# Performance work log

Measured on AMD Instinct MI355X. Metric: run time of the kernel, lower is better.

The kernel has to match this reference:

```python
import jax, jax.numpy as jnp
import numpy as np

E, H, L, DFF, PF = 256, 8, 6, 1024, 6

def _ln(x, s, b):
    m = x.mean(-1, keepdims=True)
    v = jnp.mean((x - m) ** 2, -1, keepdims=True)
    return (x - m) / jnp.sqrt(v + 1e-5) * s + b

def _gelu(x):
    return jax.nn.gelu(x, approximate=False)

def setup_inputs() -> dict:
    key = jax.random.key(0)
    ks = iter(jax.random.split(key, 40))
    B, N = 16, 512
    w = lambda shape: jax.random.normal(next(ks), shape, jnp.float32) * 0.02
    hits = jax.random.normal(next(ks), (B, N, 5), jnp.float32)
    mask = jax.random.uniform(next(ks), (B, N)) < 0.9
    mask = mask.at[:, 0].set(True)  # at least one valid hit per event
    params = jax.random.normal(next(ks), (B, 5), jnp.float32)
    return dict(
        hits=hits, mask=mask, params=params,
        embed_w=w((5, E)), embed_b=jnp.zeros(E), embed_ln_s=jnp.ones(E), embed_ln_b=jnp.zeros(E),
        pos_w=w((2, E)), pos_b=jnp.zeros(E),
        qkv_w=w((L, E, 3 * E)), out_w=w((L, E, E)), out_b=jnp.zeros((L, E)),
        pair_w1=w((L, PF, E)), pair_b1=jnp.zeros((L, E)), pair_w2=w((L, E, H)), pair_b2=jnp.zeros((L, H)),
        ffn_w1=w((L, E, DFF)), ffn_b1=jnp.zeros((L, DFF)), ffn_w2=w((L, DFF, E)), ffn_b2=jnp.zeros((L, E)),
        n1_s=jnp.ones((L, E)), n1_b=jnp.zeros((L, E)), n2_s=jnp.ones((L, E)), n2_b=jnp.zeros((L, E)),
        pfc_w1=w((5, E)), pfc_b1=jnp.zeros(E), pfc_ln_s=jnp.ones(E), pfc_ln_b=jnp.zeros(E),
        pfc_w2=w((E, E)), pfc_b2=jnp.zeros(E),
        cls_w1=w((3 * E, 512)), cls_b1=jnp.zeros(512),
        cls_w2=w((512, 256)), cls_b2=jnp.zeros(256),
        cls_w3=w((256, 2)), cls_b3=jnp.zeros(2))

def reference(hits, mask, params, embed_w, embed_b, embed_ln_s, embed_ln_b, pos_w, pos_b,
              qkv_w, out_w, out_b, pair_w1, pair_b1, pair_w2, pair_b2,
              ffn_w1, ffn_b1, ffn_w2, ffn_b2, n1_s, n1_b, n2_s, n2_b,
              pfc_w1, pfc_b1, pfc_ln_s, pfc_ln_b, pfc_w2, pfc_b2,
              cls_w1, cls_b1, cls_w2, cls_b2, cls_w3, cls_b3):
    B, N, _ = hits.shape
    pos = hits[..., :2]
    feat = _gelu(_ln(hits @ embed_w + embed_b, embed_ln_s, embed_ln_b)) + _gelu(pos @ pos_w + pos_b)

    # pairwise geometric features [B,N,N,5]
    d = hits[:, :, None, :] - hits[:, None, :, :]
    dx, dy, dr, dpe, ddt = (d[..., i] for i in range(5))
    dist = jnp.sqrt(dx * dx + dy * dy + 1e-6)
    nrm = lambda t: t / (jnp.mean(jnp.abs(t), axis=(1, 2), keepdims=True) + 1e-6)
    dist_n = dist / (jnp.mean(dist, axis=(1, 2), keepdims=True) + 1e-6)
    pair_feat = jnp.stack([nrm(dx), nrm(dy), dist_n, nrm(dr), nrm(dpe), nrm(ddt)], axis=-1)

    Dh = feat.shape[-1] // H
    scale = Dh ** -0.5
    key_mask = mask[:, None, None, :]  # [B,1,1,N]
    for l in range(qkv_w.shape[0]):
        q, k, v = jnp.split(feat @ qkv_w[l], 3, axis=-1)
        q = q.reshape(B, N, H, Dh)
        k = k.reshape(B, N, H, Dh)
        v = v.reshape(B, N, H, Dh)
        logits = jnp.einsum('bqhd,bkhd->bhqk', q, k) * scale
        bias = jax.nn.relu(pair_feat @ pair_w1[l] + pair_b1[l]) @ pair_w2[l] + pair_b2[l]  # [B,N,N,H]
        logits = logits + jnp.transpose(bias, (0, 3, 1, 2))
        logits = jnp.where(key_mask, logits, -1e9)
        attn = jax.nn.softmax(logits, axis=-1)
        out = jnp.einsum('bhqk,bkhd->bqhd', attn, v).reshape(B, N, -1)
        out = out @ out_w[l] + out_b[l]
        x = _ln(feat + out, n1_s[l], n1_b[l])
        x2 = _gelu(x @ ffn_w1[l] + ffn_b1[l]) @ ffn_w2[l] + ffn_b2[l]
        feat = _ln(x + x2, n2_s[l], n2_b[l])

    mask_f = mask[..., None].astype(feat.dtype)
    mean_feat = (feat * mask_f).sum(1) / (mask_f.sum(1) + 1e-6)
    max_feat = jnp.where(mask[..., None], feat, -1e9).max(1)
    invalid = mask.sum(1) == 0
    max_feat = jnp.where(invalid[:, None], mean_feat, max_feat)

    pf = _gelu(params @ pfc_w1 + pfc_b1)
    pf = _ln(pf, pfc_ln_s, pfc_ln_b)
    pf = _gelu(pf @ pfc_w2 + pfc_b2)

    h = jnp.concatenate([max_feat, mean_feat, pf], axis=1)
    h = _gelu(h @ cls_w1 + cls_b1)
    h = _gelu(h @ cls_w2 + cls_b2)
    return h @ cls_w3 + cls_b3
```

## Files before the change

### kernel.cpp

```cpp
#include <hip/hip_runtime.h>
#include <hip/hip_bf16.h>

#define B_ 16
#define N_ 512
#define E_ 256
#define H_ 8
#define DH_ 32
#define L_ 6
#define DFF_ 1024
#define LSN 528

typedef unsigned short ushort_t;
typedef __attribute__((ext_vector_type(8))) short short8v;
typedef __attribute__((ext_vector_type(4))) float f32x4;

__device__ __forceinline__ float bf2f_raw(unsigned short u){
    unsigned int x = ((unsigned int)u) << 16; float f;
    __builtin_memcpy(&f, &x, 4); return f;
}
__device__ __forceinline__ unsigned short f2bf_rne(float f){
    unsigned int u; __builtin_memcpy(&u, &f, 4);
    u += 0x7fffu + ((u >> 16) & 1u);
    return (unsigned short)(u >> 16);
}
__device__ __forceinline__ unsigned int packbf2(float a, float b){
    return (unsigned int)f2bf_rne(a) | ((unsigned int)f2bf_rne(b) << 16);
}
__device__ __forceinline__ unsigned int pack_hi16(float a, float b){
    unsigned int ua, ub;
    __builtin_memcpy(&ua, &a, 4); __builtin_memcpy(&ub, &b, 4);
    return __builtin_amdgcn_perm(ub, ua, 0x07060302);
}
__device__ __forceinline__ float gelu_f(float x){
    return 0.5f * x * (1.0f + erff(x * 0.7071067811865476f));
}

__global__ void detect_and_mask(const unsigned int* __restrict__ lnS_raw,
                                const void* __restrict__ mask_raw,
                                int* __restrict__ flag, int* __restrict__ maskI){
    __shared__ int s_isbf, s_m32;
    if (threadIdx.x == 0){
        s_isbf = (lnS_raw[0] == 0x3F803F80u) ? 1 : 0;
        const unsigned int* mw = (const unsigned int*)mask_raw;
        int ok = 1;
        for (int k = 0; k < 64; k++){ if (mw[k] > 1u){ ok = 0; break; } }
        s_m32 = ok;
        *flag = s_isbf;
    }
    __syncthreads();
    if (s_m32){
        const int* mi = (const int*)mask_raw;
        for (int i = threadIdx.x; i < B_*N_; i += blockDim.x) maskI[i] = (mi[i] != 0);
    } else {
        const unsigned char* mb = (const unsigned char*)mask_raw;
        for (int i = threadIdx.x; i < B_*N_; i += blockDim.x) maskI[i] = (mb[i] != 0);
    }
}

struct CvtTable {
    const void* src[36];
    int off[37];
    int dstoff[36];
};

__global__ __launch_bounds__(256) void cvt_all(CvtTable t, float* __restrict__ base,
                                               const int* __restrict__ flag){
    int gi = blockIdx.x * 256 + threadIdx.x;
    if (gi >= t.off[36]) return;
    int seg = 0;
    for (int s = 1; s < 36; s++) if (gi >= t.off[s]) seg = s;
    int loc = gi - t.off[seg];
    float* dst = base + t.dstoff[seg] + loc;
    if (*flag) *dst = bf2f_raw(((const unsigned short*)t.src[seg])[loc]);
    else       *dst = ((const float*)t.src[seg])[loc];
}

struct TPTable {
    const float* src[24];
    ushort_t* dst[24];
    int K[24], N[24];
    int tile0[25];
};

__global__ __launch_bounds__(256) void wpack(TPTable tp){
    int bid = blockIdx.x;
    int m = 0;
    while (m + 1 < 24 && bid >= tp.tile0[m+1]) m++;
    int t = bid - tp.tile0[m];
    int tiles_n = tp.N[m] >> 5;
    int tk = t / tiles_n, tn = t - tk*tiles_n;
    __shared__ float tile[32][33];
    int tx = threadIdx.x & 31, ty = threadIdx.x >> 5;
    const float* src = tp.src[m];
    int Nn = tp.N[m], Kk = tp.K[m];
    #pragma unroll
    for (int r = 0; r < 4; r++){
        int k = tk*32 + ty + r*8;
        tile[ty + r*8][tx] = src[(size_t)k*Nn + tn*32 + tx];
    }
    __syncthreads();
    ushort_t* dst = tp.dst[m];
    #pragma unroll
    for (int r = 0; r < 4; r++){
        int n = tn*32 + ty + r*8;
        dst[(size_t)n*Kk + tk*32 + tx] = f2bf_rne(tile[tx][ty + r*8]);
    }
}

__global__ __launch_bounds__(256) void pair_stats(const float* __restrict__ hits,
                                                  float* __restrict__ ppart){
    int blk = blockIdx.x;
    int b = blk >> 5, chunk = blk & 31;
    int tid = threadIdx.x;
    float acc[6] = {0,0,0,0,0,0};
    for (int ii = 0; ii < 16; ii++){
        int i = chunk*16 + ii;
        const float* hi = hits + (size_t)(b*N_ + i)*5;
        float h0=hi[0], h1=hi[1], h2=hi[2], h3=hi[3], h4=hi[4];
        for (int j = tid; j < N_; j += 256){
            const float* hj = hits + (size_t)(b*N_ + j)*5;
            float dx = h0 - hj[0], dy = h1 - hj[1];
            acc[0] += fabsf(dx);
            acc[1] += fabsf(dy);
            acc[2] += sqrtf(dx*dx + dy*dy + 1e-6f);
            acc[3] += fabsf(h2 - hj[2]);
            acc[4] += fabsf(h3 - hj[3]);
            acc[5] += fabsf(h4 - hj[4]);
        }
    }
    __shared__ float red[256];
    for (int c = 0; c < 6; c++){
        red[tid] = acc[c]; __syncthreads();
        for (int s = 128; s > 0; s >>= 1){ if (tid < s) red[tid] += red[tid+s]; __syncthreads(); }
        if (tid == 0) ppart[(size_t)(b*32 + chunk)*6 + c] = red[0];
        __syncthreads();
    }
}

__global__ void pair_fin(const float* __restrict__ ppart, float* __restrict__ pscale){
    int t = threadIdx.x;
    if (t >= B_*6) return;
    int b = t / 6, c = t % 6;
    float s = 0.f;
    for (int k = 0; k < 32; k++) s += ppart[(size_t)(b*32 + k)*6 + c];
    float mean = s * (1.0f / (float)(N_*N_));
    pscale[t] = 1.0f / (mean + 1e-6f);
}

__global__ __launch_bounds__(256) void embed_kernel(const float* __restrict__ hits,
        const float* __restrict__ ew, const float* __restrict__ eb,
        const float* __restrict__ lns, const float* __restrict__ lnb,
        const float* __restrict__ pw, const float* __restrict__ pb,
        float* __restrict__ feat, ushort_t* __restrict__ featb){
    int row = blockIdx.x; int e = threadIdx.x;
    const float* h = hits + (size_t)row*5;
    float h0=h[0], h1=h[1], h2=h[2], h3=h[3], h4=h[4];
    float t = eb[e] + h0*ew[e] + h1*ew[E_+e] + h2*ew[2*E_+e] + h3*ew[3*E_+e] + h4*ew[4*E_+e];
    __shared__ float red[256];
    red[e] = t; __syncthreads();
    for (int s = 128; s > 0; s >>= 1){ if (e < s) red[e] += red[e+s]; __syncthreads(); }
    float m = red[0] * (1.0f/E_); __syncthreads();
    float d = t - m;
    red[e] = d*d; __syncthreads();
    for (int s = 128; s > 0; s >>= 1){ if (e < s) red[e] += red[e+s]; __syncthreads(); }
    float v = red[0] * (1.0f/E_);
    float ln = d * rsqrtf(v + 1e-5f) * lns[e] + lnb[e];
    float g1 = gelu_f(ln);
    float p = pb[e] + h0*pw[e] + h1*pw[E_+e];
    float o = g1 + gelu_f(p);
    feat[(size_t)row*E_ + e] = o;
    featb[(size_t)row*E_ + e] = f2bf_rne(o);
}

template<int ACT>
__global__ __launch_bounds__(256) void gemm_bf16(const ushort_t* __restrict__ A,
        const ushort_t* __restrict__ WT, const float* __restrict__ bias,
        float* __restrict__ C, ushort_t* __restrict__ Cbf, int M, int Ncols, int K){
    __shared__ __align__(16) ushort_t As[64][72];
    __shared__ __align__(16) ushort_t Bs[64][72];
    int tid = threadIdx.x;
    int mBase = blockIdx.y * 64, nBase = blockIdx.x * 64;
    int l = tid & 63, w = tid >> 6;
    int l15 = l & 15, lg = l >> 4;
    int wm = w >> 1, wn = w & 1;
    int srow = tid >> 2, skq = (tid & 3) * 16;
    f32x4 acc00 = {0.f,0.f,0.f,0.f}, acc01 = acc00, acc10 = acc00, acc11 = acc00;
    for (int kt = 0; kt < K; kt += 64){
        uint4 av0 = *(const uint4*)(A  + (size_t)(mBase+srow)*K + kt + skq);
        uint4 av1 = *(const uint4*)(A  + (size_t)(mBase+srow)*K + kt + skq + 8);
        uint4 bv0 = *(const uint4*)(WT + (size_t)(nBase+srow)*K + kt + skq);
        uint4 bv1 = *(const uint4*)(WT + (size_t)(nBase+srow)*K + kt + skq + 8);
        *(uint4*)&As[srow][skq]     = av0;
        *(uint4*)&As[srow][skq + 8] = av1;
        *(uint4*)&Bs[srow][skq]     = bv0;
        *(uint4*)&Bs[srow][skq + 8] = bv1;
        __syncthreads();
        #pragma unroll
        for (int ks = 0; ks < 2; ks++){
            short8v a0 = *(short8v*)&As[wm*32      + l15][ks*32 + lg*8];
            short8v a1 = *(short8v*)&As[wm*32 + 16 + l15][ks*32 + lg*8];
            short8v b0 = *(short8v*)&Bs[wn*32      + l15][ks*32 + lg*8];
            short8v b1 = *(short8v*)&Bs[wn*32 + 16 + l15][ks*32 + lg*8];
            acc00 = __builtin_amdgcn_mfma_f32_16x16x32_bf16(a0, b0, acc00, 0, 0, 0);
            acc01 = __builtin_amdgcn_mfma_f32_16x16x32_bf16(a0, b1, acc01, 0, 0, 0);
            acc10 = __builtin_amdgcn_mfma_f32_16x16x32_bf16(a1, b0, acc10, 0, 0, 0);
            acc11 = __builtin_amdgcn_mfma_f32_16x16x32_bf16(a1, b1, acc11, 0, 0, 0);
        }
        __syncthreads();
    }
    #pragma unroll
    for (int fm = 0; fm < 2; fm++){
        #pragma unroll
        for (int fn = 0; fn < 2; fn++){
            f32x4 a = (fm==0) ? ((fn==0)?acc00:acc01) : ((fn==0)?acc10:acc11);
            int col = nBase + wn*32 + fn*16 + l15;
            float bs = bias ? bias[col] : 0.f;
            #pragma unroll
            for (int r = 0; r < 4; r++){
                int row = mBase + wm*32 + fm*16 + lg*4 + r;
                float o = a[r] + bs;
                if (ACT == 1) o = gelu_f(o);
                if (C)   C[(size_t)row*Ncols + col] = o;
                if (Cbf) Cbf[(size_t)row*Ncols + col] = f2bf_rne(o);
            }
        }
    }
}

__global__ __launch_bounds__(128) void pk_pack(const float* __restrict__ qkv,
        const float* __restrict__ hits, const float* __restrict__ pscale,
        const float* __restrict__ w1, unsigned int* __restrict__ PTbf,
        unsigned int* __restrict__ Kbf){
    int row = blockIdx.x;
    int b = row >> 9;
    int t = threadIdx.x;
    const float* sc6 = pscale + b*6;
    const float* h = hits + (size_t)row*5;
    float a0 = h[0]*sc6[0], a1 = h[1]*sc6[1], a2 = h[2]*sc6[3], a3 = h[3]*sc6[4], a4 = h[4]*sc6[5];
    int c0 = t*2;
    float p0 = a0*w1[c0]   + a1*w1[E_+c0]   + a2*w1[3*E_+c0]   + a3*w1[4*E_+c0]   + a4*w1[5*E_+c0];
    float p1 = a0*w1[c0+1] + a1*w1[E_+c0+1] + a2*w1[3*E_+c0+1] + a3*w1[4*E_+c0+1] + a4*w1[5*E_+c0+1];
    PTbf[(size_t)row*128 + t] = packbf2(p0, p1);
    const float* kr = qkv + (size_t)row*768 + 256 + c0;
    Kbf[(size_t)row*128 + t] = packbf2(kr[0], kr[1]);
}

__device__ __forceinline__ short8v build_afrag(uint4 pt, float4 b0, float4 b1,
                                               float4 w0, float4 w1v, float dist){
    float p0 = bf2f_raw((ushort_t)(pt.x & 0xffff)), p1 = bf2f_raw((ushort_t)(pt.x >> 16));
    float p2 = bf2f_raw((ushort_t)(pt.y & 0xffff)), p3 = bf2f_raw((ushort_t)(pt.y >> 16));
    float p4 = bf2f_raw((ushort_t)(pt.z & 0xffff)), p5 = bf2f_raw((ushort_t)(pt.z >> 16));
    float p6 = bf2f_raw((ushort_t)(pt.w & 0xffff)), p7 = bf2f_raw((ushort_t)(pt.w >> 16));
    float e0 = fmaxf(fmaf(dist, w0.x,  b0.x - p0), 0.f);
    float e1 = fmaxf(fmaf(dist, w0.y,  b0.y - p1), 0.f);
    float e2 = fmaxf(fmaf(dist, w0.z,  b0.z - p2), 0.f);
    float e3 = fmaxf(fmaf(dist, w0.w,  b0.w - p3), 0.f);
    float e4 = fmaxf(fmaf(dist, w1v.x, b1.x - p4), 0.f);
    float e5 = fmaxf(fmaf(dist, w1v.y, b1.y - p5), 0.f);
    float e6 = fmaxf(fmaf(dist, w1v.z, b1.z - p6), 0.f);
    float e7 = fmaxf(fmaf(dist, w1v.w, b1.w - p7), 0.f);
    uint4 u;
    u.x = pack_hi16(e0, e1); u.y = pack_hi16(e2, e3);
    u.z = pack_hi16(e4, e5); u.w = pack_hi16(e6, e7);
    return *(short8v*)&u;
}

__global__ __launch_bounds__(512, 4) void attn7_kernel(
        const float* __restrict__ qkv, const unsigned int* __restrict__ PTbf,
        const unsigned int* __restrict__ Kbf, const float* __restrict__ hits,
        const int* __restrict__ maskI, const float* __restrict__ pscale,
        const float* __restrict__ b1, const float* __restrict__ w1,
        const float* __restrict__ w2, const float* __restrict__ b2,
        ushort_t* __restrict__ attnob){
    __shared__ __align__(16) ushort_t Ls[2][H_][LSN];
    __shared__ __align__(16) float4 w2f[8][64];
    __shared__ float baseS[2][E_];
    __shared__ float w1dS[E_];
    __shared__ float distS[2][N_];
    __shared__ unsigned char mS[N_];
    __shared__ float b2S[8];
    __shared__ float red[512];
    __shared__ float inv_s[2][H_];

    int bx = blockIdx.x;
    int b = bx >> 8;
    int i0 = (bx & 255) * 2;
    int tid = threadIdx.x;
    int l = tid & 63, w = tid >> 6;
    int l15 = l & 15, lg = l >> 4;
    const float scale = 0.17677669529663687f;

    {
        int q = tid >> 8, c = tid & 255;
        const float* sc6 = pscale + b*6;
        const float* hr = hits + (size_t)(b*N_ + i0 + q)*5;
        float p = hr[0]*sc6[0]*w1[c] + hr[1]*sc6[1]*w1[E_+c] + hr[2]*sc6[3]*w1[3*E_+c]
                + hr[3]*sc6[4]*w1[4*E_+c] + hr[4]*sc6[5]*w1[5*E_+c];
        baseS[q][c] = p + b1[c];
        if (tid < 256) w1dS[tid] = sc6[2] * w1[2*E_ + tid];
        if (tid < 8)   b2S[tid] = b2[tid];
    }
    {
        int ks = tid >> 6, lv = tid & 63;
        int h = lv & 15, g = lv >> 4;
        uint4 u = {0u,0u,0u,0u};
        if (h < 8){
            int cb = ks*32 + g*8;
            const float* wp = w2 + (size_t)cb*H_ + h;
            u.x = packbf2(wp[0*H_], wp[1*H_]);
            u.y = packbf2(wp[2*H_], wp[3*H_]);
            u.z = packbf2(wp[4*H_], wp[5*H_]);
            u.w = packbf2(wp[6*H_], wp[7*H_]);
        }
        w2f[ks][lv] = *(float4*)&u;
    }
    for (int idx = tid; idx < 1024; idx += 512){
        int q = idx >> 9, j = idx & 511;
        const float* hi = hits + (size_t)(b*N_ + i0 + q)*5;
        const float* hj = hits + (size_t)(b*N_ + j)*5;
        float dx = hi[0] - hj[0], dy = hi[1] - hj[1];
        distS[q][j] = sqrtf(dx*dx + dy*dy + 1e-6f);
        if (q == 0) mS[j] = (unsigned char)(maskI[b*N_ + j] != 0);
    }
    uint4 qz = {0u,0u,0u,0u};
    short8v zero8 = *(short8v*)&qz;
    short8v qreg0 = zero8, qreg1 = zero8;
    if (l15 < 8){
        const float* Q0 = qkv + (size_t)(b*N_ + i0    )*768 + l15*32 + lg*8;
        const float* Q1 = qkv + (size_t)(b*N_ + i0 + 1)*768 + l15*32 + lg*8;
        uint4 u0, u1;
        u0.x = packbf2(Q0[0]*scale, Q0[1]*scale); u0.y = packbf2(Q0[2]*scale, Q0[3]*scale);
        u0.z = packbf2(Q0[4]*scale, Q0[5]*scale); u0.w = packbf2(Q0[6]*scale, Q0[7]*scale);
        u1.x = packbf2(Q1[0]*scale, Q1[1]*scale); u1.y = packbf2(Q1[2]*scale, Q1[3]*scale);
        u1.z = packbf2(Q1[4]*scale, Q1[5]*scale); u1.w = packbf2(Q1[6]*scale, Q1[7]*scale);
        qreg0 = *(short8v*)&u0; qreg1 = *(short8v*)&u1;
    }
    __syncthreads();

    int jb = w << 6;
    int j0 = jb + l15;
    const unsigned int* PTb = PTbf + (size_t)b*N_*128;
    const unsigned int* Kb  = Kbf  + (size_t)b*N_*128;
    f32x4 a00 = {0.f,0.f,0.f,0.f}, a01 = a00, a02 = a00, a03 = a00;
    f32x4 a10 = a00, a11 = a00, a12 = a00, a13 = a00;
    float d00 = distS[0][j0], d01 = distS[0][j0+16], d02 = distS[0][j0+32], d03 = distS[0][j0+48];
    float d10 = distS[1][j0], d11 = distS[1][j0+16], d12 = distS[1][j0+32], d13 = distS[1][j0+48];

    #pragma unroll
    for (int ks = 0; ks < 8; ks++){
        int cbase = ks*32 + lg*8;
        float4 wfrag4 = w2f[ks][l];
        short8v wfrag = *(short8v*)&wfrag4;
        float4 w0  = *(float4*)&w1dS[cbase];
        float4 w1v = *(float4*)&w1dS[cbase + 4];
        uint4 pt0 = *(const uint4*)(PTb + (size_t)(j0      )*128 + (cbase >> 1));
        uint4 pt1 = *(const uint4*)(PTb + (size_t)(j0 + 16 )*128 + (cbase >> 1));
        uint4 pt2 = *(const uint4*)(PTb + (size_t)(j0 + 32 )*128 + (cbase >> 1));
        uint4 pt3 = *(const uint4*)(PTb + (size_t)(j0 + 48 )*128 + (cbase >> 1));
        {
            float4 bs0 = *(float4*)&baseS[0][cbase];
            float4 bs1 = *(float4*)&baseS[0][cbase + 4];
            short8v f0 = build_afrag(pt0, bs0, bs1, w0, w1v, d00);
            short8v f1 = build_afrag(pt1, bs0, bs1, w0, w1v, d01);
            short8v f2 = build_afrag(pt2, bs0, bs1, w0, w1v, d02);
            short8v f3 = build_afrag(pt3, bs0, bs1, w0, w1v, d03);
            a00 = __builtin_amdgcn_mfma_f32_16x16x32_bf16(f0, wfrag, a00, 0, 0, 0);
            a01 = __builtin_amdgcn_mfma_f32_16x16x32_bf16(f1, wfrag, a01, 0, 0, 0);
            a02 = __builtin_amdgcn_mfma_f32_16x16x32_bf16(f2, wfrag, a02, 0, 0, 0);
            a03 = __builtin_amdgcn_mfma_f32_16x16x32_bf16(f3, wfrag, a03, 0, 0, 0);
        }
        {
            float4 bs0 = *(float4*)&baseS[1][cbase];
            float4 bs1 = *(float4*)&baseS[1][cbase + 4];
            short8v f0 = build_afrag(pt0, bs0, bs1, w0, w1v, d10);
            short8v f1 = build_afrag(pt1, bs0, bs1, w0, w1v, d11);
            short8v f2 = build_afrag(pt2, bs0, bs1, w0, w1v, d12);
            short8v f3 = build_afrag(pt3, bs0, bs1, w0, w1v, d13);
            a10 = __builtin_amdgcn_mfma_f32_16x16x32_bf16(f0, wfrag, a10, 0, 0, 0);
            a11 = __builtin_amdgcn_mfma_f32_16x16x32_bf16(f1, wfrag, a11, 0, 0, 0);
            a12 = __builtin_amdgcn_mfma_f32_16x16x32_bf16(f2, wfrag, a12, 0, 0, 0);
            a13 = __builtin_amdgcn_mfma_f32_16x16x32_bf16(f3, wfrag, a13, 0, 0, 0);
        }
    }
    #pragma unroll
    for (int ks = 0; ks < 8; ks++){
        int dbase = ks*32 + lg*8;
        short8v q0f = (l15 == ks) ? qreg0 : zero8;
        short8v q1f = (l15 == ks) ? qreg1 : zero8;
        uint4 k0 = *(const uint4*)(Kb + (size_t)(j0      )*128 + (dbase >> 1));
        uint4 k1 = *(const uint4*)(Kb + (size_t)(j0 + 16 )*128 + (dbase >> 1));
        uint4 k2 = *(const uint4*)(Kb + (size_t)(j0 + 32 )*128 + (dbase >> 1));
        uint4 k3 = *(const uint4*)(Kb + (size_t)(j0 + 48 )*128 + (dbase >> 1));
        short8v kf0 = *(short8v*)&k0, kf1 = *(short8v*)&k1, kf2 = *(short8v*)&k2, kf3 = *(short8v*)&k3;
        a00 = __builtin_amdgcn_mfma_f32_16x16x32_bf16(kf0, q0f, a00, 0, 0, 0);
        a01 = __builtin_amdgcn_mfma_f32_16x16x32_bf16(kf1, q0f, a01, 0, 0, 0);
        a02 = __builtin_amdgcn_mfma_f32_16x16x32_bf16(kf2, q0f, a02, 0, 0, 0);
        a03 = __builtin_amdgcn_mfma_f32_16x16x32_bf16(kf3, q0f, a03, 0, 0, 0);
        a10 = __builtin_amdgcn_mfma_f32_16x16x32_bf16(kf0, q1f, a10, 0, 0, 0);
        a11 = __builtin_amdgcn_mfma_f32_16x16x32_bf16(kf1, q1f, a11, 0, 0, 0);
        a12 = __builtin_amdgcn_mfma_f32_16x16x32_bf16(kf2, q1f, a12, 0, 0, 0);
        a13 = __builtin_amdgcn_mfma_f32_16x16x32_bf16(kf3, q1f, a13, 0, 0, 0);
    }

    if (l15 < 8){
        float b2h = b2S[l15];
        ushort_t neg = f2bf_rne(-1e9f);
        #pragma unroll
        for (int r = 0; r < 4; r++){
            int jr0 = jb +  0 + lg*4 + r;
            int jr1 = jb + 16 + lg*4 + r;
            int jr2 = jb + 32 + lg*4 + r;
            int jr3 = jb + 48 + lg*4 + r;
            Ls[0][l15][jr0] = mS[jr0] ? f2bf_rne(a00[r] + b2h) : neg;
            Ls[0][l15][jr1] = mS[jr1] ? f2bf_rne(a01[r] + b2h) : neg;
            Ls[0][l15][jr2] = mS[jr2] ? f2bf_rne(a02[r] + b2h) : neg;
            Ls[0][l15][jr3] = mS[jr3] ? f2bf_rne(a03[r] + b2h) : neg;
            Ls[1][l15][jr0] = mS[jr0] ? f2bf_rne(a10[r] + b2h) : neg;
            Ls[1][l15][jr1] = mS[jr1] ? f2bf_rne(a11[r] + b2h) : neg;
            Ls[1][l15][jr2] = mS[jr2] ? f2bf_rne(a12[r] + b2h) : neg;
            Ls[1][l15][jr3] = mS[jr3] ? f2bf_rne(a13[r] + b2h) : neg;
        }
    }
    __syncthreads();

    {
        int g = tid >> 5, lane = tid & 31;
        int sq = g >> 3, shh = g & 7;
        ushort_t* Li = &Ls[sq][shh][0];
        float m = -3e38f;
        for (int jj = lane; jj < N_; jj += 32) m = fmaxf(m, bf2f_raw(Li[jj]));
        red[tid] = m; __syncthreads();
        #pragma unroll
        for (int s = 16; s > 0; s >>= 1){ if (lane < s) red[tid] = fmaxf(red[tid], red[tid+s]); __syncthreads(); }
        float mh = red[g << 5]; __syncthreads();
        float ss = 0.f;
        for (int jj = lane; jj < N_; jj += 32){
            float e = __expf(bf2f_raw(Li[jj]) - mh);
            ushort_t us = f2bf_rne(e);
            Li[jj] = us;
            ss += bf2f_raw(us);
        }
        red[tid] = ss; __syncthreads();
        #pragma unroll
        for (int s = 16; s > 0; s >>= 1){ if (lane < s) red[tid] += red[tid+s]; __syncthreads(); }
        if (lane == 0) inv_s[sq][shh] = 1.0f / red[g << 5];
        __syncthreads();
    }

    {
        int q = tid >> 8, d = tid & 255, hh = d >> 5;
        const float* vb = qkv + (size_t)(b*N_)*768 + 512 + d;
        const uint4* Lp = (const uint4*)&Ls[q][hh][0];
        float o = 0.f;
        for (int jb2 = 0; jb2 < N_/8; jb2++){
            uint4 ww = Lp[jb2];
            int j0b = jb2*8;
            unsigned int wk[4] = {ww.x, ww.y, ww.z, ww.w};
            #pragma unroll
            for (int k = 0; k < 4; k++){
                unsigned int lo = wk[k] << 16;
                unsigned int hi = wk[k] & 0xffff0000u;
                float plo, phi;
                __builtin_memcpy(&plo, &lo, 4);
                __builtin_memcpy(&phi, &hi, 4);
                o = fmaf(plo, vb[(size_t)(j0b + 2*k    )*768], o);
                o = fmaf(phi, vb[(size_t)(j0b + 2*k + 1)*768], o);
            }
        }
        attnob[(size_t)(b*N_ + i0 + q)*E_ + d] = f2bf_rne(o * inv_s[q][hh]);
    }
}

__global__ __launch_bounds__(256) void ln_add_kernel(const float* __restrict__ a,
        const float* __restrict__ bsrc, const float* __restrict__ s,
        const float* __restrict__ bb, float* __restrict__ out,
        ushort_t* __restrict__ outb){
    int row = blockIdx.x, e = threadIdx.x;
    float v = a[(size_t)row*E_ + e] + bsrc[(size_t)row*E_ + e];
    __shared__ float red[256];
    red[e] = v; __syncthreads();
    for (int t = 128; t > 0; t >>= 1){ if (e < t) red[e] += red[e+t]; __syncthreads(); }
    float m = red[0] * (1.0f/E_); __syncthreads();
    float d = v - m;
    red[e] = d*d; __syncthreads();
    for (int t = 128; t > 0; t >>= 1){ if (e < t) red[e] += red[e+t]; __syncthreads(); }
    float var = red[0] * (1.0f/E_);
    float o = d * rsqrtf(var + 1e-5f) * s[e] + bb[e];
    out[(size_t)row*E_ + e] = o;
    outb[(size_t)row*E_ + e] = f2bf_rne(o);
}

__global__ __launch_bounds__(256) void pool_kernel(const float* __restrict__ feat,
        const int* __restrict__ maskI, float* __restrict__ pooled){
    int b = blockIdx.x, e = threadIdx.x;
    __shared__ int ml[N_];
    for (int n = e; n < N_; n += 256) ml[n] = maskI[b*N_ + n];
    __syncthreads();
    float s = 0.f, mx = -1e30f; int cnt = 0;
    for (int n = 0; n < N_; n++){
        if (ml[n]){
            float v = feat[(size_t)(b*N_ + n)*E_ + e];
            s += v; mx = fmaxf(mx, v); cnt++;
        }
    }
    float mean = s / ((float)cnt + 1e-6f);
    if (cnt == 0) mx = mean;
    pooled[b*768 + e]       = mx;
    pooled[b*768 + 256 + e] = mean;
}

__global__ __launch_bounds__(256) void pf_kernel(const float* __restrict__ params,
        const float* __restrict__ w1, const float* __restrict__ b1,
        const float* __restrict__ lns, const float* __restrict__ lnb,
        const float* __restrict__ w2, const float* __restrict__ b2,
        float* __restrict__ pooled){
    int b = blockIdx.x, e = threadIdx.x;
    __shared__ float red[256];
    __shared__ float pfn[256];
    float p0 = params[b*5+0], p1 = params[b*5+1], p2 = params[b*5+2], p3 = params[b*5+3], p4 = params[b*5+4];
    float t = b1[e] + p0*w1[e] + p1*w1[E_+e] + p2*w1[2*E_+e] + p3*w1[3*E_+e] + p4*w1[4*E_+e];
    t = gelu_f(t);
    red[e] = t; __syncthreads();
    for (int s = 128; s > 0; s >>= 1){ if (e < s) red[e] += red[e+s]; __syncthreads(); }
    float m = red[0] * (1.0f/E_); __syncthreads();
    float d = t - m;
    red[e] = d*d; __syncthreads();
    for (int s = 128; s > 0; s >>= 1){ if (e < s) red[e] += red[e+s]; __syncthreads(); }
    float v = red[0] * (1.0f/E_);
    pfn[e] = d * rsqrtf(v + 1e-5f) * lns[e] + lnb[e];
    __syncthreads();
    float u = b2[e];
    for (int c = 0; c < E_; c++) u += pfn[c] * w2[c*E_ + e];
    pooled[b*768 + 512 + e] = gelu_f(u);
}

__global__ __launch_bounds__(512) void cls_kernel(const float* __restrict__ pooled,
        const float* __restrict__ w1, const float* __restrict__ b1,
        const float* __restrict__ w2, const float* __restrict__ b2,
        const float* __restrict__ w3, const float* __restrict__ b3,
        float* __restrict__ out){
    int b = blockIdx.x, t = threadIdx.x;
    __shared__ float hb[768];
    __shared__ float h1[512];
    __shared__ float h2[256];
    for (int idx = t; idx < 768; idx += 512) hb[idx] = pooled[b*768 + idx];
    __syncthreads();
    float a = b1[t];
    for (int c = 0; c < 768; c++) a += hb[c] * w1[c*512 + t];
    h1[t] = gelu_f(a);
    __syncthreads();
    if (t < 256){
        float a2 = b2[t];
        for (int c = 0; c < 512; c++) a2 += h1[c] * w2[c*256 + t];
        h2[t] = gelu_f(a2);
    }
    __syncthreads();
    if (t < 2){
        float a3 = b3[t];
        for (int c = 0; c < 256; c++) a3 += h2[c] * w3[c*2 + t];
        out[b*2 + t] = a3;
    }
}

extern "C" void kernel_launch(void* const* d_in, const int* in_sizes, int n_in,
                              void* d_out, int out_size, void* d_ws, size_t ws_size,
                              hipStream_t stream){
    enum { I_HITS=0, I_MASK=1, I_PARAMS=2, I_EMBED_W=3, I_EMBED_B=4, I_ELN_S=5, I_ELN_B=6,
           I_POS_W=7, I_POS_B=8, I_QKV_W=9, I_OUT_W=10, I_OUT_B=11, I_PW1=12, I_PB1=13,
           I_PW2=14, I_PB2=15, I_FW1=16, I_FB1=17, I_FW2=18, I_FB2=19, I_N1S=20, I_N1B=21,
           I_N2S=22, I_N2B=23, I_PFW1=24, I_PFB1=25, I_PFLS=26, I_PFLB=27, I_PFW2=28, I_PFB2=29,
           I_CW1=30, I_CB1=31, I_CW2=32, I_CB2=33, I_CW3=34, I_CB3=35 };
    (void)n_in; (void)out_size; (void)ws_size;

    float* wsf = (float*)d_ws;
    int* maskI = (int*)d_ws;
    int* flag  = (int*)d_ws + 8192;
    size_t off = 8448;

    CvtTable tbl;
    float* cv[36];
    for (int idx = 0; idx < 36; idx++){
        if (idx == I_MASK){ cv[idx] = nullptr; tbl.src[idx] = d_in[idx]; tbl.dstoff[idx] = 0; continue; }
        cv[idx] = wsf + off;
        tbl.src[idx] = d_in[idx];
        tbl.dstoff[idx] = (int)off;
        off += (size_t)in_sizes[idx];
        off = (off + 3) & ~(size_t)3;
    }
    {
        int c2 = 0;
        for (int idx = 0; idx < 36; idx++){
            tbl.off[idx] = c2;
            if (idx != I_MASK) c2 += in_sizes[idx];
        }
        tbl.off[36] = c2;
    }

    float* feat  = wsf + off; off += (size_t)B_*N_*E_;
    float* qkv   = wsf + off; off += (size_t)B_*N_*3*E_;
    float* xbuf  = wsf + off; off += (size_t)B_*N_*E_;
    float* tmp   = wsf + off; off += (size_t)B_*N_*E_;
    float* ppart = wsf + off; off += (size_t)B_*32*6;
    float* pscale= wsf + off; off += (size_t)B_*6 + 2;
    float* pooled= wsf + off; off += (size_t)B_*768;
    ushort_t* featb  = (ushort_t*)(wsf + off); off += (size_t)B_*N_*E_/2;
    ushort_t* xbufb  = (ushort_t*)(wsf + off); off += (size_t)B_*N_*E_/2;
    ushort_t* attnob = (ushort_t*)(wsf + off); off += (size_t)B_*N_*E_/2;
    ushort_t* ffnhb  = (ushort_t*)(wsf + off); off += (size_t)B_*N_*DFF_/2;
    ushort_t* wtq = (ushort_t*)(wsf + off); off += (size_t)L_*768*E_/2;
    ushort_t* wto = (ushort_t*)(wsf + off); off += (size_t)L_*E_*E_/2;
    ushort_t* wt1 = (ushort_t*)(wsf + off); off += (size_t)L_*DFF_*E_/2;
    ushort_t* wt2 = (ushort_t*)(wsf + off); off += (size_t)L_*E_*DFF_/2;
    unsigned int* PTbf = (unsigned int*)tmp;
    unsigned int* Kbf  = PTbf + (size_t)B_*N_*128;

    detect_and_mask<<<1, 256, 0, stream>>>((const unsigned int*)d_in[I_ELN_S], d_in[I_MASK], flag, maskI);
    {
        int total = tbl.off[36];
        cvt_all<<<(total + 255)/256, 256, 0, stream>>>(tbl, wsf, flag);
    }

    {
        TPTable tp;
        int t0 = 0;
        for (int l = 0; l < L_; l++){
            int m = l*4;
            tp.src[m+0] = cv[I_QKV_W] + (size_t)l*E_*3*E_; tp.dst[m+0] = wtq + (size_t)l*768*E_;
            tp.K[m+0] = E_;   tp.N[m+0] = 3*E_;
            tp.src[m+1] = cv[I_OUT_W] + (size_t)l*E_*E_;   tp.dst[m+1] = wto + (size_t)l*E_*E_;
            tp.K[m+1] = E_;   tp.N[m+1] = E_;
            tp.src[m+2] = cv[I_FW1] + (size_t)l*E_*DFF_;   tp.dst[m+2] = wt1 + (size_t)l*DFF_*E_;
            tp.K[m+2] = E_;   tp.N[m+2] = DFF_;
            tp.src[m+3] = cv[I_FW2] + (size_t)l*DFF_*E_;   tp.dst[m+3] = wt2 + (size_t)l*E_*DFF_;
            tp.K[m+3] = DFF_; tp.N[m+3] = E_;
        }
        for (int m = 0; m < 24; m++){
            tp.tile0[m] = t0;
            t0 += (tp.K[m] >> 5) * (tp.N[m] >> 5);
        }
        tp.tile0[24] = t0;
        wpack<<<t0, 256, 0, stream>>>(tp);
    }

    pair_stats<<<B_*32, 256, 0, stream>>>(cv[I_HITS], ppart);
    pair_fin<<<1, 128, 0, stream>>>(ppart, pscale);
    embed_kernel<<<B_*N_, 256, 0, stream>>>(cv[I_HITS], cv[I_EMBED_W], cv[I_EMBED_B],
                                            cv[I_ELN_S], cv[I_ELN_B], cv[I_POS_W], cv[I_POS_B],
                                            feat, featb);

    for (int l = 0; l < L_; l++){
        gemm_bf16<0><<<dim3(12,128), 256, 0, stream>>>(featb, wtq + (size_t)l*768*E_,
                                                       nullptr, qkv, nullptr, B_*N_, 3*E_, E_);
        pk_pack<<<B_*N_, 128, 0, stream>>>(qkv, cv[I_HITS], pscale,
                                           cv[I_PW1] + (size_t)l*6*E_, PTbf, Kbf);
        attn7_kernel<<<B_*(N_/2), 512, 0, stream>>>(qkv, PTbf, Kbf, cv[I_HITS], maskI, pscale,
                                               cv[I_PB1] + (size_t)l*E_,
                                               cv[I_PW1] + (size_t)l*6*E_,
                                               cv[I_PW2] + (size_t)l*E_*H_,
                                               cv[I_PB2] + (size_t)l*H_,
                                               attnob);
        gemm_bf16<0><<<dim3(4,128), 256, 0, stream>>>(attnob, wto + (size_t)l*E_*E_,
                                                      cv[I_OUT_B] + (size_t)l*E_, tmp, nullptr,
                                                      B_*N_, E_, E_);
        ln_add_kernel<<<B_*N_, 256, 0, stream>>>(feat, tmp, cv[I_N1S] + (size_t)l*E_,
                                                 cv[I_N1B] + (size_t)l*E_, xbuf, xbufb);
        gemm_bf16<1><<<dim3(16,128), 256, 0, stream>>>(xbufb, wt1 + (size_t)l*DFF_*E_,
                                                       cv[I_FB1] + (size_t)l*DFF_, nullptr, ffnhb,
                                                       B_*N_, DFF_, E_);
        gemm_bf16<0><<<dim3(4,128), 256, 0, stream>>>(ffnhb, wt2 + (size_t)l*E_*DFF_,
                                                      cv[I_FB2] + (size_t)l*E_, tmp, nullptr,
                                                      B_*N_, E_, DFF_);
        ln_add_kernel<<<B_*N_, 256, 0, stream>>>(xbuf, tmp, cv[I_N2S] + (size_t)l*E_,
                                                 cv[I_N2B] + (size_t)l*E_, feat, featb);
    }

    pool_kernel<<<B_, 256, 0, stream>>>(feat, maskI, pooled);
    pf_kernel<<<B_, 256, 0, stream>>>(cv[I_PARAMS], cv[I_PFW1], cv[I_PFB1],
                                      cv[I_PFLS], cv[I_PFLB], cv[I_PFW2], cv[I_PFB2], pooled);
    cls_kernel<<<B_, 512, 0, stream>>>(pooled, cv[I_CW1], cv[I_CB1], cv[I_CW2], cv[I_CB2],
                                       cv[I_CW3], cv[I_CB3], (float*)d_out);
}
```

Before: 3.388 ms.

## Switch pair-bias MLP to packed fp16 math and transpose V to fp16

The pair-bias hidden layer is now computed with packed half2 FMA/max instead of per-element fp32 ops plus bf16 packing, and uses fp16 MFMA. Attention logits and probabilities are stored as fp16. A new vT_pack kernel writes a transposed fp16 copy of V, so the PV accumulation does contiguous vector loads with fdot2 instead of strided fp32 gathers. This cuts ALU and memory traffic in the attention kernel. It adds an extra kernel launch per layer and risks fp16 range and precision problems in the intermediate values.

```diff
diff --git a/kernel.cpp b/kernel.cpp
--- a/kernel.cpp
+++ b/kernel.cpp
@@ -1,5 +1,6 @@
 #include <hip/hip_runtime.h>
 #include <hip/hip_bf16.h>
+#include <hip/hip_fp16.h>
 
 #define B_ 16
 #define N_ 512
@@ -13,6 +14,8 @@
 typedef unsigned short ushort_t;
 typedef __attribute__((ext_vector_type(8))) short short8v;
 typedef __attribute__((ext_vector_type(4))) float f32x4;
+typedef __attribute__((ext_vector_type(2))) _Float16 half2v;
+typedef __attribute__((ext_vector_type(8))) _Float16 half8v;
 
 __device__ __forceinline__ float bf2f_raw(unsigned short u){
     unsigned int x = ((unsigned int)u) << 16; float f;
@@ -26,10 +29,24 @@
 __device__ __forceinline__ unsigned int packbf2(float a, float b){
     return (unsigned int)f2bf_rne(a) | ((unsigned int)f2bf_rne(b) << 16);
 }
-__device__ __forceinline__ unsigned int pack_hi16(float a, float b){
-    unsigned int ua, ub;
-    __builtin_memcpy(&ua, &a, 4); __builtin_memcpy(&ub, &b, 4);
-    return __builtin_amdgcn_perm(ub, ua, 0x07060302);
+__device__ __forceinline__ half2v u2hv(unsigned int u){ half2v h; __builtin_memcpy(&h, &u, 4); return h; }
+__device__ __forceinline__ unsigned int hv2u(half2v h){ unsigned int u; __builtin_memcpy(&u, &h, 4); return u; }
+__device__ __forceinline__ unsigned int pack2h(float a, float b){
+    half2v h; h.x = (_Float16)a; h.y = (_Float16)b; return hv2u(h);
+}
+__device__ __forceinline__ ushort_t f2h_u(float f){
+    _Float16 h = (_Float16)f; ushort_t u; __builtin_memcpy(&u, &h, 2); return u;
+}
+__device__ __forceinline__ float h2f_u(ushort_t u){
+    _Float16 h; __builtin_memcpy(&h, &u, 2); return (float)h;
+}
+__device__ __forceinline__ float dot2h(unsigned int p, unsigned int v, float c){
+#if __has_builtin(__builtin_amdgcn_fdot2)
+    return __builtin_amdgcn_fdot2(u2hv(p), u2hv(v), c, false);
+#else
+    half2v a = u2hv(p), b = u2hv(v);
+    return fmaf((float)a.y, (float)b.y, fmaf((float)a.x, (float)b.x, c));
+#endif
 }
 __device__ __forceinline__ float gelu_f(float x){
     return 0.5f * x * (1.0f + erff(x * 0.7071067811865476f));
@@ -104,6 +121,25 @@
     for (int r = 0; r < 4; r++){
         int n = tn*32 + ty + r*8;
         dst[(size_t)n*Kk + tk*32 + tx] = f2bf_rne(tile[tx][ty + r*8]);
+    }
+}
+
+__global__ __launch_bounds__(256) void vT_pack(const float* __restrict__ qkv,
+                                               ushort_t* __restrict__ VTf){
+    __shared__ float t[32][33];
+    int b = blockIdx.z;
+    int n0 = blockIdx.x * 32, d0 = blockIdx.y * 32;
+    int tx = threadIdx.x & 31, ty = threadIdx.x >> 5;
+    #pragma unroll
+    for (int r = 0; r < 4; r++){
+        int n = ty + r*8;
+        t[n][tx] = qkv[(size_t)(b*N_ + n0 + n)*768 + 512 + d0 + tx];
+    }
+    __syncthreads();
+    #pragma unroll
+    for (int r = 0; r < 4; r++){
+        int d = ty + r*8;
+        VTf[(size_t)(b*E_ + d0 + d)*N_ + n0 + tx] = f2h_u(t[tx][d]);
     }
 }
 
@@ -229,7 +265,7 @@
 
 __global__ __launch_bounds__(128) void pk_pack(const float* __restrict__ qkv,
         const float* __restrict__ hits, const float* __restrict__ pscale,
-        const float* __restrict__ w1, unsigned int* __restrict__ PTbf,
+        const float* __restrict__ w1, unsigned int* __restrict__ PThf,
         unsigned int* __restrict__ Kbf){
     int row = blockIdx.x;
     int b = row >> 9;
@@ -240,42 +276,38 @@
     int c0 = t*2;
     float p0 = a0*w1[c0]   + a1*w1[E_+c0]   + a2*w1[3*E_+c0]   + a3*w1[4*E_+c0]   + a4*w1[5*E_+c0];
     float p1 = a0*w1[c0+1] + a1*w1[E_+c0+1] + a2*w1[3*E_+c0+1] + a3*w1[4*E_+c0+1] + a4*w1[5*E_+c0+1];
-    PTbf[(size_t)row*128 + t] = packbf2(p0, p1);
+    PThf[(size_t)row*128 + t] = pack2h(p0, p1);
     const float* kr = qkv + (size_t)row*768 + 256 + c0;
     Kbf[(size_t)row*128 + t] = packbf2(kr[0], kr[1]);
 }
 
-__device__ __forceinline__ short8v build_afrag(uint4 pt, float4 b0, float4 b1,
-                                               float4 w0, float4 w1v, float dist){
-    float p0 = bf2f_raw((ushort_t)(pt.x & 0xffff)), p1 = bf2f_raw((ushort_t)(pt.x >> 16));
-    float p2 = bf2f_raw((ushort_t)(pt.y & 0xffff)), p3 = bf2f_raw((ushort_t)(pt.y >> 16));
-    float p4 = bf2f_raw((ushort_t)(pt.z & 0xffff)), p5 = bf2f_raw((ushort_t)(pt.z >> 16));
-    float p6 = bf2f_raw((ushort_t)(pt.w & 0xffff)), p7 = bf2f_raw((ushort_t)(pt.w >> 16));
-    float e0 = fmaxf(fmaf(dist, w0.x,  b0.x - p0), 0.f);
-    float e1 = fmaxf(fmaf(dist, w0.y,  b0.y - p1), 0.f);
-    float e2 = fmaxf(fmaf(dist, w0.z,  b0.z - p2), 0.f);
-    float e3 = fmaxf(fmaf(dist, w0.w,  b0.w - p3), 0.f);
-    float e4 = fmaxf(fmaf(dist, w1v.x, b1.x - p4), 0.f);
-    float e5 = fmaxf(fmaf(dist, w1v.y, b1.y - p5), 0.f);
-    float e6 = fmaxf(fmaf(dist, w1v.z, b1.z - p6), 0.f);
-    float e7 = fmaxf(fmaf(dist, w1v.w, b1.w - p7), 0.f);
+__device__ __forceinline__ half8v build_afrag_h(uint4 pt, uint4 bs, uint4 wd, half2v d2){
+    half2v z2 = (half2v)(_Float16)0;
+    half2v r0 = d2 * u2hv(wd.x) + (u2hv(bs.x) - u2hv(pt.x));
+    half2v r1 = d2 * u2hv(wd.y) + (u2hv(bs.y) - u2hv(pt.y));
+    half2v r2 = d2 * u2hv(wd.z) + (u2hv(bs.z) - u2hv(pt.z));
+    half2v r3 = d2 * u2hv(wd.w) + (u2hv(bs.w) - u2hv(pt.w));
+    r0 = __builtin_elementwise_max(r0, z2);
+    r1 = __builtin_elementwise_max(r1, z2);
+    r2 = __builtin_elementwise_max(r2, z2);
+    r3 = __builtin_elementwise_max(r3, z2);
     uint4 u;
-    u.x = pack_hi16(e0, e1); u.y = pack_hi16(e2, e3);
-    u.z = pack_hi16(e4, e5); u.w = pack_hi16(e6, e7);
-    return *(short8v*)&u;
-}
-
-__global__ __launch_bounds__(512, 4) void attn7_kernel(
-        const float* __restrict__ qkv, const unsigned int* __restrict__ PTbf,
-        const unsigned int* __restrict__ Kbf, const float* __restrict__ hits,
+    u.x = hv2u(r0); u.y = hv2u(r1); u.z = hv2u(r2); u.w = hv2u(r3);
+    half8v r; __builtin_memcpy(&r, &u, 16); return r;
+}
+
+__global__ __launch_bounds__(512, 4) void attn8_kernel(
+        const float* __restrict__ qkv, const unsigned int* __restrict__ PThf,
+        const unsigned int* __restrict__ Kbf, const ushort_t* __restrict__ VTf,
+        const float* __restrict__ hits,
         const int* __restrict__ maskI, const float* __restrict__ pscale,
         const float* __restrict__ b1, const float* __restrict__ w1,
         const float* __restrict__ w2, const float* __restrict__ b2,
         ushort_t* __restrict__ attnob){
     __shared__ __align__(16) ushort_t Ls[2][H_][LSN];
-    __shared__ __align__(16) float4 w2f[8][64];
-    __shared__ float baseS[2][E_];
-    __shared__ float w1dS[E_];
+    __shared__ __align__(16) uint4 w2f[8][64];
+    __shared__ __align__(16) unsigned int baseH[2][128];
+    __shared__ __align__(16) unsigned int w1dH[128];
     __shared__ float distS[2][N_];
     __shared__ unsigned char mS[N_];
     __shared__ float b2S[8];
@@ -290,15 +322,21 @@
     int l15 = l & 15, lg = l >> 4;
     const float scale = 0.17677669529663687f;
 
-    {
-        int q = tid >> 8, c = tid & 255;
+    if (tid < 256){
+        int q = tid >> 7, cp = tid & 127;
+        int c = cp*2;
         const float* sc6 = pscale + b*6;
         const float* hr = hits + (size_t)(b*N_ + i0 + q)*5;
-        float p = hr[0]*sc6[0]*w1[c] + hr[1]*sc6[1]*w1[E_+c] + hr[2]*sc6[3]*w1[3*E_+c]
-                + hr[3]*sc6[4]*w1[4*E_+c] + hr[4]*sc6[5]*w1[5*E_+c];
-        baseS[q][c] = p + b1[c];
-        if (tid < 256) w1dS[tid] = sc6[2] * w1[2*E_ + tid];
-        if (tid < 8)   b2S[tid] = b2[tid];
+        float pa = hr[0]*sc6[0]*w1[c] + hr[1]*sc6[1]*w1[E_+c] + hr[2]*sc6[3]*w1[3*E_+c]
+                 + hr[3]*sc6[4]*w1[4*E_+c] + hr[4]*sc6[5]*w1[5*E_+c] + b1[c];
+        float pb2 = hr[0]*sc6[0]*w1[c+1] + hr[1]*sc6[1]*w1[E_+c+1] + hr[2]*sc6[3]*w1[3*E_+c+1]
+                  + hr[3]*sc6[4]*w1[4*E_+c+1] + hr[4]*sc6[5]*w1[5*E_+c+1] + b1[c+1];
+        baseH[q][cp] = pack2h(pa, pb2);
+        if (tid < 128){
+            float wa = sc6[2]*w1[2*E_ + c], wb = sc6[2]*w1[2*E_ + c + 1];
+            w1dH[cp] = pack2h(wa, wb);
+        }
+        if (tid < 8) b2S[tid] = b2[tid];
     }
     {
         int ks = tid >> 6, lv = tid & 63;
@@ -307,12 +345,12 @@
         if (h < 8){
             int cb = ks*32 + g*8;
             const float* wp = w2 + (size_t)cb*H_ + h;
-            u.x = packbf2(wp[0*H_], wp[1*H_]);
-            u.y = packbf2(wp[2*H_], wp[3*H_]);
-            u.z = packbf2(wp[4*H_], wp[5*H_]);
-            u.w = packbf2(wp[6*H_], wp[7*H_]);
-        }
-        w2f[ks][lv] = *(float4*)&u;
+            u.x = pack2h(wp[0*H_], wp[1*H_]);
+            u.y = pack2h(wp[2*H_], wp[3*H_]);
+            u.z = pack2h(wp[4*H_], wp[5*H_]);
+            u.w = pack2h(wp[6*H_], wp[7*H_]);
+        }
+        w2f[ks][lv] = u;
     }
     for (int idx = tid; idx < 1024; idx += 512){
         int q = idx >> 9, j = idx & 511;
@@ -339,47 +377,50 @@
 
     int jb = w << 6;
     int j0 = jb + l15;
-    const unsigned int* PTb = PTbf + (size_t)b*N_*128;
+    const unsigned int* PTb = PThf + (size_t)b*N_*128;
     const unsigned int* Kb  = Kbf  + (size_t)b*N_*128;
     f32x4 a00 = {0.f,0.f,0.f,0.f}, a01 = a00, a02 = a00, a03 = a00;
     f32x4 a10 = a00, a11 = a00, a12 = a00, a13 = a00;
-    float d00 = distS[0][j0], d01 = distS[0][j0+16], d02 = distS[0][j0+32], d03 = distS[0][j0+48];
-    float d10 = distS[1][j0], d11 = distS[1][j0+16], d12 = distS[1][j0+32], d13 = distS[1][j0+48];
+    half2v e00 = (half2v)(_Float16)distS[0][j0];
+    half2v e01 = (half2v)(_Float16)distS[0][j0+16];
+    half2v e02 = (half2v)(_Float16)distS[0][j0+32];
+    half2v e03 = (half2v)(_Float16)distS[0][j0+48];
+    half2v e10 = (half2v)(_Float16)distS[1][j0];
+    half2v e11 = (half2v)(_Float16)distS[1][j0+16];
+    half2v e12 = (half2v)(_Float16)distS[1][j0+32];
+    half2v e13 = (half2v)(_Float16)distS[1][j0+48];
 
     #pragma unroll
     for (int ks = 0; ks < 8; ks++){
         int cbase = ks*32 + lg*8;
-        float4 wfrag4 = w2f[ks][l];
-        short8v wfrag = *(short8v*)&wfrag4;
-        float4 w0  = *(float4*)&w1dS[cbase];
-        float4 w1v = *(float4*)&w1dS[cbase + 4];
+        uint4 wfrag4 = w2f[ks][l];
+        half8v wfrag; __builtin_memcpy(&wfrag, &wfrag4, 16);
+        uint4 wd = *(uint4*)&w1dH[cbase >> 1];
         uint4 pt0 = *(const uint4*)(PTb + (size_t)(j0      )*128 + (cbase >> 1));
         uint4 pt1 = *(const uint4*)(PTb + (size_t)(j0 + 16 )*128 + (cbase >> 1));
         uint4 pt2 = *(const uint4*)(PTb + (size_t)(j0 + 32 )*128 + (cbase >> 1));
         uint4 pt3 = *(const uint4*)(PTb + (size_t)(j0 + 48 )*128 + (cbase >> 1));
         {
-            float4 bs0 = *(float4*)&baseS[0][cbase];
-            float4 bs1 = *(float4*)&baseS[0][cbase + 4];
-            short8v f0 = build_afrag(pt0, bs0, bs1, w0, w1v, d00);
-            short8v f1 = build_afrag(pt1, bs0, bs1, w0, w1v, d01);
-            short8v f2 = build_afrag(pt2, bs0, bs1, w0, w1v, d02);
-            short8v f3 = build_afrag(pt3, bs0, bs1, w0, w1v, d03);
-            a00 = __builtin_amdgcn_mfma_f32_16x16x32_bf16(f0, wfrag, a00, 0, 0, 0);
-            a01 = __builtin_amdgcn_mfma_f32_16x16x32_bf16(f1, wfrag, a01, 0, 0, 0);
-            a02 = __builtin_amdgcn_mfma_f32_16x16x32_bf16(f2, wfrag, a02, 0, 0, 0);
-            a03 = __builtin_amdgcn_mfma_f32_16x16x32_bf16(f3, wfrag, a03, 0, 0, 0);
+            uint4 bs = *(uint4*)&baseH[0][cbase >> 1];
+            half8v f0 = build_afrag_h(pt0, bs, wd, e00);
+            half8v f1 = build_afrag_h(pt1, bs, wd, e01);
+            half8v f2 = build_afrag_h(pt2, bs, wd, e02);
+            half8v f3 = build_afrag_h(pt3, bs, wd, e03);
+            a00 = __builtin_amdgcn_mfma_f32_16x16x32_f16(f0, wfrag, a00, 0, 0, 0);
+            a01 = __builtin_amdgcn_mfma_f32_16x16x32_f16(f1, wfrag, a01, 0, 0, 0);
+            a02 = __builtin_amdgcn_mfma_f32_16x16x32_f16(f2, wfrag, a02, 0, 0, 0);
+            a03 = __builtin_amdgcn_mfma_f32_16x16x32_f16(f3, wfrag, a03, 0, 0, 0);
         }
         {
-            float4 bs0 = *(float4*)&baseS[1][cbase];
-            float4 bs1 = *(float4*)&baseS[1][cbase + 4];
-            short8v f0 = build_afrag(pt0, bs0, bs1, w0, w1v, d10);
-            short8v f1 = build_afrag(pt1, bs0, bs1, w0, w1v, d11);
-            short8v f2 = build_afrag(pt2, bs0, bs1, w0, w1v, d12);
-            short8v f3 = build_afrag(pt3, bs0, bs1, w0, w1v, d13);
-            a10 = __builtin_amdgcn_mfma_f32_16x16x32_bf16(f0, wfrag, a10, 0, 0, 0);
-            a11 = __builtin_amdgcn_mfma_f32_16x16x32_bf16(f1, wfrag, a11, 0, 0, 0);
-            a12 = __builtin_amdgcn_mfma_f32_16x16x32_bf16(f2, wfrag, a12, 0, 0, 0);
-            a13 = __builtin_amdgcn_mfma_f32_16x16x32_bf16(f3, wfrag, a13, 0, 0, 0);
+            uint4 bs = *(uint4*)&baseH[1][cbase >> 1];
+            half8v f0 = build_afrag_h(pt0, bs, wd, e10);
+            half8v f1 = build_afrag_h(pt1, bs, wd, e11);
+            half8v f2 = build_afrag_h(pt2, bs, wd, e12);
+            half8v f3 = build_afrag_h(pt3, bs, wd, e13);
+            a10 = __builtin_amdgcn_mfma_f32_16x16x32_f16(f0, wfrag, a10, 0, 0, 0);
+            a11 = __builtin_amdgcn_mfma_f32_16x16x32_f16(f1, wfrag, a11, 0, 0, 0);
+            a12 = __builtin_amdgcn_mfma_f32_16x16x32_f16(f2, wfrag, a12, 0, 0, 0);
+            a13 = __builtin_amdgcn_mfma_f32_16x16x32_f16(f3, wfrag, a13, 0, 0, 0);
         }
     }
     #pragma unroll
@@ -404,21 +445,21 @@
 
     if (l15 < 8){
         float b2h = b2S[l15];
-        ushort_t neg = f2bf_rne(-1e9f);
+        ushort_t neg = f2h_u(-1e9f);
         #pragma unroll
         for (int r = 0; r < 4; r++){
             int jr0 = jb +  0 + lg*4 + r;
             int jr1 = jb + 16 + lg*4 + r;
             int jr2 = jb + 32 + lg*4 + r;
             int jr3 = jb + 48 + lg*4 + r;
-            Ls[0][l15][jr0] = mS[jr0] ? f2bf_rne(a00[r] + b2h) : neg;
-            Ls[0][l15][jr1] = mS[jr1] ? f2bf_rne(a01[r] + b2h) : neg;
-            Ls[0][l15][jr2] = mS[jr2] ? f2bf_rne(a02[r] + b2h) : neg;
-            Ls[0][l15][jr3] = mS[jr3] ? f2bf_rne(a03[r] + b2h) : neg;
-            Ls[1][l15][jr0] = mS[jr0] ? f2bf_rne(a10[r] + b2h) : neg;
-            Ls[1][l15][jr1] = mS[jr1] ? f2bf_rne(a11[r] + b2h) : neg;
-            Ls[1][l15][jr2] = mS[jr2] ? f2bf_rne(a12[r] + b2h) : neg;
-            Ls[1][l15][jr3] = mS[jr3] ? f2bf_rne(a13[r] + b2h) : neg;
+            Ls[0][l15][jr0] = mS[jr0] ? f2h_u(a00[r] + b2h) : neg;
+            Ls[0][l15][jr1] = mS[jr1] ? f2h_u(a01[r] + b2h) : neg;
+            Ls[0][l15][jr2] = mS[jr2] ? f2h_u(a02[r] + b2h) : neg;
+            Ls[0][l15][jr3] = mS[jr3] ? f2h_u(a03[r] + b2h) : neg;
+            Ls[1][l15][jr0] = mS[jr0] ? f2h_u(a10[r] + b2h) : neg;
+            Ls[1][l15][jr1] = mS[jr1] ? f2h_u(a11[r] + b2h) : neg;
+            Ls[1][l15][jr2] = mS[jr2] ? f2h_u(a12[r] + b2h) : neg;
+            Ls[1][l15][jr3] = mS[jr3] ? f2h_u(a13[r] + b2h) : neg;
         }
     }
     __syncthreads();
@@ -428,17 +469,17 @@
         int sq = g >> 3, shh = g & 7;
         ushort_t* Li = &Ls[sq][shh][0];
         float m = -3e38f;
-        for (int jj = lane; jj < N_; jj += 32) m = fmaxf(m, bf2f_raw(Li[jj]));
+        for (int jj = lane; jj < N_; jj += 32) m = fmaxf(m, h2f_u(Li[jj]));
         red[tid] = m; __syncthreads();
         #pragma unroll
         for (int s = 16; s > 0; s >>= 1){ if (lane < s) red[tid] = fmaxf(red[tid], red[tid+s]); __syncthreads(); }
         float mh = red[g << 5]; __syncthreads();
         float ss = 0.f;
         for (int jj = lane; jj < N_; jj += 32){
-            float e = __expf(bf2f_raw(Li[jj]) - mh);
-            ushort_t us = f2bf_rne(e);
+            float e = __expf(h2f_u(Li[jj]) - mh);
+            ushort_t us = f2h_u(e);
             Li[jj] = us;
-            ss += bf2f_raw(us);
+            ss += h2f_u(us);
         }
         red[tid] = ss; __syncthreads();
         #pragma unroll
@@ -449,23 +490,18 @@
 
     {
         int q = tid >> 8, d = tid & 255, hh = d >> 5;
-        const float* vb = qkv + (size_t)(b*N_)*768 + 512 + d;
+        const unsigned int* vtrow = (const unsigned int*)(VTf + (size_t)(b*E_ + d)*N_);
+        const uint4* vp = (const uint4*)vtrow;
         const uint4* Lp = (const uint4*)&Ls[q][hh][0];
         float o = 0.f;
-        for (int jb2 = 0; jb2 < N_/8; jb2++){
-            uint4 ww = Lp[jb2];
-            int j0b = jb2*8;
-            unsigned int wk[4] = {ww.x, ww.y, ww.z, ww.w};
-            #pragma unroll
-            for (int k = 0; k < 4; k++){
-                unsigned int lo = wk[k] << 16;
-                unsigned int hi = wk[k] & 0xffff0000u;
-                float plo, phi;
-                __builtin_memcpy(&plo, &lo, 4);
-                __builtin_memcpy(&phi, &hi, 4);
-                o = fmaf(plo, vb[(size_t)(j0b + 2*k    )*768], o);
-                o = fmaf(phi, vb[(size_t)(j0b + 2*k + 1)*768], o);
-            }
+        #pragma unroll 4
+        for (int t2 = 0; t2 < N_/8; t2++){
+            uint4 vv = vp[t2];
+            uint4 pp = Lp[t2];
+            o = dot2h(pp.x, vv.x, o);
+            o = dot2h(pp.y, vv.y, o);
+            o = dot2h(pp.z, vv.z, o);
+            o = dot2h(pp.w, vv.w, o);
         }
         attnob[(size_t)(b*N_ + i0 + q)*E_ + d] = f2bf_rne(o * inv_s[q][hh]);
     }
@@ -607,12 +643,13 @@
     ushort_t* xbufb  = (ushort_t*)(wsf + off); off += (size_t)B_*N_*E_/2;
     ushort_t* attnob = (ushort_t*)(wsf + off); off += (size_t)B_*N_*E_/2;
     ushort_t* ffnhb  = (ushort_t*)(wsf + off); off += (size_t)B_*N_*DFF_/2;
+    ushort_t* VTf    = (ushort_t*)(wsf + off); off += (size_t)B_*E_*N_/2;
     ushort_t* wtq = (ushort_t*)(wsf + off); off += (size_t)L_*768*E_/2;
     ushort_t* wto = (ushort_t*)(wsf + off); off += (size_t)L_*E_*E_/2;
     ushort_t* wt1 = (ushort_t*)(wsf + off); off += (size_t)L_*DFF_*E_/2;
     ushort_t* wt2 = (ushort_t*)(wsf + off); off += (size_t)L_*E_*DFF_/2;
-    unsigned int* PTbf = (unsigned int*)tmp;
-    unsigned int* Kbf  = PTbf + (size_t)B_*N_*128;
+    unsigned int* PThf = (unsigned int*)tmp;
+    unsigned int* Kbf  = PThf + (size_t)B_*N_*128;
 
     detect_and_mask<<<1, 256, 0, stream>>>((const unsigned int*)d_in[I_ELN_S], d_in[I_MASK], flag, maskI);
     {
@@ -652,8 +689,9 @@
         gemm_bf16<0><<<dim3(12,128), 256, 0, stream>>>(featb, wtq + (size_t)l*768*E_,
                                                        nullptr, qkv, nullptr, B_*N_, 3*E_, E_);
         pk_pack<<<B_*N_, 128, 0, stream>>>(qkv, cv[I_HITS], pscale,
-                                           cv[I_PW1] + (size_t)l*6*E_, PTbf, Kbf);
-        attn7_kernel<<<B_*(N_/2), 512, 0, stream>>>(qkv, PTbf, Kbf, cv[I_HITS], maskI, pscale,
+                                           cv[I_PW1] + (size_t)l*6*E_, PThf, Kbf);
+        vT_pack<<<dim3(16,8,16), 256, 0, stream>>>(qkv, VTf);
+        attn8_kernel<<<B_*(N_/2), 512, 0, stream>>>(qkv, PThf, Kbf, VTf, cv[I_HITS], maskI, pscale,
                                                cv[I_PB1] + (size_t)l*E_,
                                                cv[I_PW1] + (size_t)l*6*E_,
                                                cv[I_PW2] + (size_t)l*E_*H_,
```

Result: slower. 3.663 ms (+8.1%).
